# Performance work log

Measured on AMD Instinct MI355X. Metric: run time of the kernel, lower is better.

The kernel has to match this reference:

```python
import jax, jax.numpy as jnp
import numpy as np
from jax import lax

I, H, D1 = 130, 10, 20  # input_size, hidden_size, linear1 width


def _gru_last(x, Wih, Whh, bih, bhh):
    """PyTorch-convention GRU (gate order r,z,n); returns last hidden state [B,H]."""
    # Precompute input projections for all timesteps: [B,T,3H]
    xi = jnp.einsum('bti,gi->btg', x, Wih) + bih
    h0 = jnp.zeros((x.shape[0], H), x.dtype)

    def step(h, xt):  # xt: [B,3H]
        gh = h @ Whh.T + bhh  # [B,3H]
        r = jax.nn.sigmoid(xt[:, :H] + gh[:, :H])
        z = jax.nn.sigmoid(xt[:, H:2 * H] + gh[:, H:2 * H])
        n = jnp.tanh(xt[:, 2 * H:] + r * gh[:, 2 * H:])
        h_new = (1.0 - z) * n + z * h
        return h_new, None

    hT, _ = lax.scan(step, h0, jnp.swapaxes(xi, 0, 1))  # scan over time
    return hT


def setup_inputs() -> dict:
    key = jax.random.key(0)
    ks = jax.random.split(key, 12)
    B, T = 2048, 128
    s_ih = 1.0 / np.sqrt(H)
    inp = {
        'ru': jax.random.normal(ks[0], (B, T, I), jnp.float32),
        'en': jax.random.normal(ks[1], (B, T, I), jnp.float32),
        'ru_Wih': jax.random.uniform(ks[2], (3 * H, I), jnp.float32, -s_ih, s_ih),
        'ru_Whh': jax.random.uniform(ks[3], (3 * H, H), jnp.float32, -s_ih, s_ih),
        'ru_bih': jax.random.uniform(ks[4], (3 * H,), jnp.float32, -s_ih, s_ih),
        'ru_bhh': jax.random.uniform(ks[5], (3 * H,), jnp.float32, -s_ih, s_ih),
        'en_Wih': jax.random.uniform(ks[6], (3 * H, I), jnp.float32, -s_ih, s_ih),
        'en_Whh': jax.random.uniform(ks[7], (3 * H, H), jnp.float32, -s_ih, s_ih),
        'en_bih': jax.random.uniform(ks[8], (3 * H,), jnp.float32, -s_ih, s_ih),
        'en_bhh': jax.random.uniform(ks[9], (3 * H,), jnp.float32, -s_ih, s_ih),
        'W1': jax.random.uniform(ks[10], (D1, 2 * H), jnp.float32, -1 / np.sqrt(2 * H), 1 / np.sqrt(2 * H)),
        'b1': jnp.zeros((D1,), jnp.float32),
        'W2': jax.random.uniform(ks[11], (1, D1), jnp.float32, -1 / np.sqrt(D1), 1 / np.sqrt(D1)),
        'b2': jnp.zeros((1,), jnp.float32),
    }
    return inp


def reference(ru, en, ru_Wih, ru_Whh, ru_bih, ru_bhh,
              en_Wih, en_Whh, en_bih, en_bhh, W1, b1, W2, b2):
    ru_h = _gru_last(ru, ru_Wih, ru_Whh, ru_bih, ru_bhh)  # [B,H] (last timestep output)
    en_h = _gru_last(en, en_Wih, en_Whh, en_bih, en_bhh)  # [B,H]
    grus_out = jnp.concatenate([ru_h, en_h], axis=1)       # [B,2H]
    h1 = grus_out @ W1.T + b1                              # [B,20] (no activation in original)
    out = h1 @ W2.T + b2                                   # [B,1]
    return out
```

## Files before the change

### kernel.cpp

```cpp
#include <hip/hip_runtime.h>
#include <hip/hip_bf16.h>


#define BB 2048
#define TT 128
#define II 130
#define ROWS_PER_GRU (BB * TT)
#define ROWS_TOTAL   (2 * ROWS_PER_GRU)

typedef __attribute__((ext_vector_type(8))) short short8v;
typedef __attribute__((ext_vector_type(4))) float f32x4;

__device__ __forceinline__ float sigmoidf_fast(float x) {
    return __fdividef(1.f, 1.f + __expf(-x));
}
__device__ __forceinline__ float tanhf_fast(float x) {
    float ax = fabsf(x);
    float e = __expf(-2.f * ax);
    float t = __fdividef(1.f - e, 1.f + e);
    return copysignf(t, x);
}

__device__ __forceinline__ void split2(float x0, float x1,
                                       unsigned& hi, unsigned& lo) {
    unsigned u0 = __float_as_uint(x0), u1 = __float_as_uint(x1);
    hi = (u0 >> 16) | (u1 & 0xffff0000u);
    float f0 = __uint_as_float(u0 & 0xffff0000u);
    float f1 = __uint_as_float(u1 & 0xffff0000u);
    unsigned l0 = __float_as_uint(x0 - f0);
    unsigned l1 = __float_as_uint(x1 - f1);
    lo = (l0 >> 16) | (l1 & 0xffff0000u);
}

union U8 { unsigned u[4]; short8v v; };

__device__ __forceinline__ void load_split(const float* __restrict__ p,
                                           short8v& hi, short8v& lo) {
    U8 H, L;
    #pragma unroll
    for (int i = 0; i < 4; ++i) {
        const float2 xy = *(const float2*)(p + 2 * i);
        split2(xy.x, xy.y, H.u[i], L.u[i]);
    }
    hi = H.v; lo = L.v;
}

__global__ __launch_bounds__(256)
void xi_gemm(const float* __restrict__ ru, const float* __restrict__ en,
             const float* __restrict__ ruWih, const float* __restrict__ rubih,
             const float* __restrict__ enWih, const float* __restrict__ enbih,
             float* __restrict__ xi)
{
    const int tid  = threadIdx.x;
    const int lane = tid & 63;
    const int lr   = lane & 15;
    const int lk   = lane >> 4;
    const int w    = blockIdx.x * 4 + (tid >> 6);
    const int gru  = (w >= 4096);
    const long row0 = (long)(w & 4095) * 64;

    const float* __restrict__ X   = gru ? en    : ru;
    const float* __restrict__ Wf  = gru ? enWih : ruWih;
    const float* __restrict__ bih = gru ? enbih : rubih;

    short8v Bhi[2][4], Blo[2][4];
    float biasv[2], wt0[2], wt1[2];
    #pragma unroll
    for (int t = 0; t < 2; ++t) {
        const int g = 16 * t + lr;
        const int gv = (g < 30) ? g : 0;
        #pragma unroll
        for (int q = 0; q < 4; ++q)
            load_split(Wf + (long)gv * II + 32 * q + 8 * lk, Bhi[t][q], Blo[t][q]);
        if (g >= 30) {
            const short8v z = {0, 0, 0, 0, 0, 0, 0, 0};
            #pragma unroll
            for (int q = 0; q < 4; ++q) { Bhi[t][q] = z; Blo[t][q] = z; }
        }
        biasv[t] = bih[gv];
        const float2 wt = *(const float2*)(Wf + (long)gv * II + 128);
        wt0[t] = wt.x; wt1[t] = wt.y;
    }

    f32x4 acc[4][2];
    #pragma unroll
    for (int m = 0; m < 4; ++m)
        #pragma unroll
        for (int t = 0; t < 2; ++t)
            acc[m][t] = (f32x4){biasv[t], biasv[t], biasv[t], biasv[t]};

    #pragma unroll
    for (int m = 0; m < 4; ++m) {
        const float* __restrict__ xr = X + (row0 + 16 * m + lr) * (long)II;
        #pragma unroll
        for (int q = 0; q < 4; ++q) {
            short8v ahi, alo;
            load_split(xr + 32 * q + 8 * lk, ahi, alo);
            acc[m][0] = __builtin_amdgcn_mfma_f32_16x16x32_bf16(ahi, Bhi[0][q], acc[m][0], 0, 0, 0);
            acc[m][0] = __builtin_amdgcn_mfma_f32_16x16x32_bf16(ahi, Blo[0][q], acc[m][0], 0, 0, 0);
            acc[m][0] = __builtin_amdgcn_mfma_f32_16x16x32_bf16(alo, Bhi[0][q], acc[m][0], 0, 0, 0);
            acc[m][1] = __builtin_amdgcn_mfma_f32_16x16x32_bf16(ahi, Bhi[1][q], acc[m][1], 0, 0, 0);
            acc[m][1] = __builtin_amdgcn_mfma_f32_16x16x32_bf16(ahi, Blo[1][q], acc[m][1], 0, 0, 0);
            acc[m][1] = __builtin_amdgcn_mfma_f32_16x16x32_bf16(alo, Bhi[1][q], acc[m][1], 0, 0, 0);
        }
    }

    const long gb = (long)gru * ROWS_PER_GRU;
    #pragma unroll
    for (int m = 0; m < 4; ++m) {
        #pragma unroll
        for (int r = 0; r < 4; ++r) {
            const long rr = row0 + 16 * m + 4 * lk + r;
            const float2 xt = *(const float2*)(X + rr * (long)II + 128);
            float* __restrict__ xo = xi + (gb + rr) * 30;
            const float v0 = acc[m][0][r] + xt.x * wt0[0] + xt.y * wt1[0];
            xo[lr] = v0;
            if (lr < 14) {
                const float v1 = acc[m][1][r] + xt.x * wt0[1] + xt.y * wt1[1];
                xo[16 + lr] = v1;
            }
        }
    }
}

__global__ __launch_bounds__(256, 4)
void gru_scan(const float* __restrict__ xi,
              const float* __restrict__ ruWhh, const float* __restrict__ rubhh,
              const float* __restrict__ enWhh, const float* __restrict__ enbhh,
              const float* __restrict__ W1, const float* __restrict__ b1,
              const float* __restrict__ W2, const float* __restrict__ b2,
              float* __restrict__ out)
{
    const int tid  = threadIdx.x;
    const int wv   = tid >> 6;
    const int lane = tid & 63;
    const int c    = lane >> 5;
    const int k    = lane & 31;
    const int kq   = (k < 10) ? k : 0;
    const int chain = (blockIdx.x * 4 + wv) * 2 + c;
    const int gru   = chain >> 11;
    const int b     = chain & (BB - 1);

    const float* __restrict__ Whh = gru ? enWhh : ruWhh;
    const float* __restrict__ bhh = gru ? enbhh : rubhh;

    float whhR[10], whhZ[10], whhN[10];
    #pragma unroll
    for (int j = 0; j < 10; ++j) {
        whhR[j] = Whh[kq * 10 + j];
        whhZ[j] = Whh[(10 + kq) * 10 + j];
        whhN[j] = Whh[(20 + kq) * 10 + j];
    }
    const float bR = bhh[kq], bZ = bhh[10 + kq], bN = bhh[20 + kq];

    __shared__ __align__(16) float lds[4][32];
    float* __restrict__ H = lds[wv] + c * 16;
    if (k < 12) H[k] = 0.f;
    float hown = 0.f;

    const float* __restrict__ xrow =
        xi + ((long)gru * ROWS_PER_GRU + (long)b * TT) * 30;

    float xR0 = xrow[kq],      xZ0 = xrow[10 + kq],  xN0 = xrow[20 + kq];
    float xR1 = xrow[30 + kq], xZ1 = xrow[40 + kq],  xN1 = xrow[50 + kq];

    for (int t = 0; t < TT; ++t) {
        const float xR = xR0, xZ = xZ0, xN = xN0;
        xR0 = xR1; xZ0 = xZ1; xN0 = xN1;
        {
            const int tn = (t + 2 < TT) ? t + 2 : TT - 1;
            const float* __restrict__ xp = xrow + (long)tn * 30;
            xR1 = xp[kq]; xZ1 = xp[10 + kq]; xN1 = xp[20 + kq];
        }

        const float4 h03 = *(const float4*)(H);
        const float4 h47 = *(const float4*)(H + 4);
        const float2 h89 = *(const float2*)(H + 8);

        float gr = bR, gz = bZ, gn = bN;
        gr = fmaf(whhR[0], h03.x, gr); gz = fmaf(whhZ[0], h03.x, gz); gn = fmaf(whhN[0], h03.x, gn);
        gr = fmaf(whhR[1], h03.y, gr); gz = fmaf(whhZ[1], h03.y, gz); gn = fmaf(whhN[1], h03.y, gn);
        gr = fmaf(whhR[2], h03.z, gr); gz = fmaf(whhZ[2], h03.z, gz); gn = fmaf(whhN[2], h03.z, gn);
        gr = fmaf(whhR[3], h03.w, gr); gz = fmaf(whhZ[3], h03.w, gz); gn = fmaf(whhN[3], h03.w, gn);
        gr = fmaf(whhR[4], h47.x, gr); gz = fmaf(whhZ[4], h47.x, gz); gn = fmaf(whhN[4], h47.x, gn);
        gr = fmaf(whhR[5], h47.y, gr); gz = fmaf(whhZ[5], h47.y, gz); gn = fmaf(whhN[5], h47.y, gn);
        gr = fmaf(whhR[6], h47.z, gr); gz = fmaf(whhZ[6], h47.z, gz); gn = fmaf(whhN[6], h47.z, gn);
        gr = fmaf(whhR[7], h47.w, gr); gz = fmaf(whhZ[7], h47.w, gz); gn = fmaf(whhN[7], h47.w, gn);
        gr = fmaf(whhR[8], h89.x, gr); gz = fmaf(whhZ[8], h89.x, gz); gn = fmaf(whhN[8], h89.x, gn);
        gr = fmaf(whhR[9], h89.y, gr); gz = fmaf(whhZ[9], h89.y, gz); gn = fmaf(whhN[9], h89.y, gn);

        const float r = sigmoidf_fast(xR + gr);
        const float z = sigmoidf_fast(xZ + gz);
        const float n = tanhf_fast(xN + r * gn);
        const float hnew = fmaf(z, hown - n, n);
        hown = hnew;
        if (k < 10) H[k] = hnew;
    }

    float val = 0.f;
    if (k < 10) {
        float v = 0.f;
        #pragma unroll
        for (int d = 0; d < 20; ++d)
            v = fmaf(W2[d], W1[d * 20 + gru * 10 + k], v);
        val = v * hown;
        if (k == 0 && gru == 0) {
            float c0 = b2[0];
            #pragma unroll
            for (int d = 0; d < 20; ++d) c0 = fmaf(W2[d], b1[d], c0);
            val += c0;
        }
    }
    val += __shfl_xor(val, 8);
    val += __shfl_xor(val, 4);
    val += __shfl_xor(val, 2);
    val += __shfl_xor(val, 1);
    if (k == 0) atomicAdd(&out[b], val);
}

__global__ __launch_bounds__(256, 4)
void gru_fused(const float* __restrict__ ru, const float* __restrict__ en,
               const float* __restrict__ ruWih, const float* __restrict__ ruWhh,
               const float* __restrict__ rubih, const float* __restrict__ rubhh,
               const float* __restrict__ enWih, const float* __restrict__ enWhh,
               const float* __restrict__ enbih, const float* __restrict__ enbhh,
               const float* __restrict__ W1, const float* __restrict__ b1,
               const float* __restrict__ W2, const float* __restrict__ b2,
               float* __restrict__ out)
{
    const int tid  = threadIdx.x;
    const int wv   = tid >> 6;
    const int lane = tid & 63;
    const int g    = lane & 31;
    const int h    = lane >> 5;
    const int wid  = blockIdx.x * 4 + wv;
    const int gru  = wid >> 11;
    const int b    = wid & (BB - 1);

    const float* __restrict__ x   = gru ? en    : ru;
    const float* __restrict__ Wih = gru ? enWih : ruWih;
    const float* __restrict__ Whh = gru ? enWhh : ruWhh;
    const float* __restrict__ bih = gru ? enbih : rubih;
    const float* __restrict__ bhh = gru ? enbhh : rubhh;

    __shared__ __align__(16) float lds[4][176];
    float* __restrict__ X    = lds[wv];
    float* __restrict__ PRE  = X + 132;
    float* __restrict__ Hbuf = X + 164;

    const int gq = (g < 30) ? g : 0;
    float wih[64];
    #pragma unroll
    for (int j = 0; j < 64; ++j) wih[j] = Wih[gq * II + h * 64 + j];
    const float w_e = Wih[gq * II + 128 + h];
    float whh[10];
    #pragma unroll
    for (int k = 0; k < 10; ++k) whh[k] = Whh[gq * 10 + k];
    const float bihg = bih[gq];
    const float bhhg = bhh[gq];

    if (lane < 12) Hbuf[lane] = 0.f;
    float hown = 0.f;

    const float* __restrict__ xrow = x + (size_t)b * (TT * II);
    float xa = xrow[lane];
    float xb = xrow[64 + lane];
    float xc = (lane < 2) ? xrow[128 + lane] : 0.f;

    for (int t = 0; t < TT; ++t) {
        X[lane] = xa;
        X[64 + lane] = xb;
        if (lane < 2) X[128 + lane] = xc;
        {
            const int tn = (t < TT - 1) ? t + 1 : t;
            const float* __restrict__ xn = xrow + (size_t)tn * II;
            xa = xn[lane];
            xb = xn[64 + lane];
            xc = (lane < 2) ? xn[128 + lane] : 0.f;
        }
        const float4 h03 = *(const float4*)(Hbuf);
        const float4 h47 = *(const float4*)(Hbuf + 4);
        const float2 h89 = *(const float2*)(Hbuf + 8);
        float gh0 = fmaf(whh[0], h03.x, bhhg);
        float gh1 = whh[1] * h03.y;
        gh0 = fmaf(whh[2], h03.z, gh0);
        gh1 = fmaf(whh[3], h03.w, gh1);
        gh0 = fmaf(whh[4], h47.x, gh0);
        gh1 = fmaf(whh[5], h47.y, gh1);
        gh0 = fmaf(whh[6], h47.z, gh0);
        gh1 = fmaf(whh[7], h47.w, gh1);
        gh0 = fmaf(whh[8], h89.x, gh0);
        gh1 = fmaf(whh[9], h89.y, gh1);
        const float gh = gh0 + gh1;

        float s0 = 0.f, s1 = 0.f, s2 = 0.f, s3 = 0.f;
        const float4* __restrict__ xb4 = (const float4*)(X + h * 64);
        #pragma unroll
        for (int c = 0; c < 16; ++c) {
            const float4 v = xb4[c];
            s0 = fmaf(wih[4 * c + 0], v.x, s0);
            s1 = fmaf(wih[4 * c + 1], v.y, s1);
            s2 = fmaf(wih[4 * c + 2], v.z, s2);
            s3 = fmaf(wih[4 * c + 3], v.w, s3);
        }
        float s = (s0 + s1) + (s2 + s3);
        s = fmaf(w_e, X[128 + h], s);
        s += __shfl_xor(s, 32);

        const float xiv = s + bihg;
        const float pre = xiv + gh;
        if (lane < 30) PRE[lane] = pre;
        const float rpre = PRE[(g - 20) & 31];
        const float zpre = PRE[(g - 10) & 31];
        const float r = sigmoidf_fast(rpre);
        const float z = sigmoidf_fast(zpre);
        const float n = tanhf_fast(xiv + r * gh);
        const float hnew = (1.f - z) * n + z * hown;
        hown = hnew;
        if (lane >= 20 && lane < 30) Hbuf[lane - 20] = hnew;
    }

    float val = 0.f;
    if (lane < 10) {
        const float hk = Hbuf[lane];
        float v = 0.f;
        #pragma unroll
        for (int d = 0; d < 20; ++d)
            v = fmaf(W2[d], W1[d * 20 + gru * 10 + lane], v);
        val = v * hk;
        if (lane == 0 && gru == 0) {
            float c0 = b2[0];
            #pragma unroll
            for (int d = 0; d < 20; ++d) c0 = fmaf(W2[d], b1[d], c0);
            val += c0;
        }
    }
    #pragma unroll
    for (int o = 32; o > 0; o >>= 1) val += __shfl_xor(val, o);
    if (lane == 0) atomicAdd(&out[b], val);
}

extern "C" void kernel_launch(void* const* d_in, const int* in_sizes, int n_in,
                              void* d_out, int out_size, void* d_ws, size_t ws_size,
                              hipStream_t stream) {
    (void)in_sizes; (void)n_in;
    const float* ru    = (const float*)d_in[0];
    const float* en    = (const float*)d_in[1];
    const float* ruWih = (const float*)d_in[2];
    const float* ruWhh = (const float*)d_in[3];
    const float* rubih = (const float*)d_in[4];
    const float* rubhh = (const float*)d_in[5];
    const float* enWih = (const float*)d_in[6];
    const float* enWhh = (const float*)d_in[7];
    const float* enbih = (const float*)d_in[8];
    const float* enbhh = (const float*)d_in[9];
    const float* W1    = (const float*)d_in[10];
    const float* b1    = (const float*)d_in[11];
    const float* W2    = (const float*)d_in[12];
    const float* b2    = (const float*)d_in[13];
    float* out = (float*)d_out;

    hipMemsetAsync(d_out, 0, (size_t)out_size * sizeof(float), stream);

    const size_t xi_bytes = (size_t)ROWS_TOTAL * 30 * sizeof(float);
    if (ws_size >= xi_bytes) {
        float* xi = (float*)d_ws;
        xi_gemm<<<dim3(2048), dim3(256), 0, stream>>>(
            ru, en, ruWih, rubih, enWih, enbih, xi);
        gru_scan<<<dim3(512), dim3(256), 0, stream>>>(
            xi, ruWhh, rubhh, enWhh, enbhh, W1, b1, W2, b2, out);
    } else {
        gru_fused<<<dim3(1024), dim3(256), 0, stream>>>(
            ru, en, ruWih, ruWhh, rubih, rubhh,
            enWih, enWhh, enbih, enbhh, W1, b1, W2, b2, out);
    }
}
```

Baseline: 142.1 us.

## Stage input rows through LDS with coalesced float4 loads and register prefetch

The input-projection GEMM now copies each 16-row tile of X into per-wave shared memory using fully coalesced float4 loads, instead of reading strided 8-float chunks straight from global memory. The next tile is prefetched into registers while the current one is computed, so global latency overlaps with the MFMA work. Tail columns are also read from LDS. The cost is 33 KB of LDS per block, which may limit occupancy, and there is no barrier between the LDS writes and reads, so correctness relies on each wave only touching its own slice.

```diff
diff --git a/kernel.cpp b/kernel.cpp
--- a/kernel.cpp
+++ b/kernel.cpp
@@ -52,10 +52,11 @@
              float* __restrict__ xi)
 {
     const int tid  = threadIdx.x;
+    const int wv   = tid >> 6;
     const int lane = tid & 63;
     const int lr   = lane & 15;
     const int lk   = lane >> 4;
-    const int w    = blockIdx.x * 4 + (tid >> 6);
+    const int w    = blockIdx.x * 4 + wv;
     const int gru  = (w >= 4096);
     const long row0 = (long)(w & 4095) * 64;
 
@@ -82,41 +83,65 @@
         wt0[t] = wt.x; wt1[t] = wt.y;
     }
 
-    f32x4 acc[4][2];
-    #pragma unroll
-    for (int m = 0; m < 4; ++m)
-        #pragma unroll
-        for (int t = 0; t < 2; ++t)
-            acc[m][t] = (f32x4){biasv[t], biasv[t], biasv[t], biasv[t]};
-
-    #pragma unroll
-    for (int m = 0; m < 4; ++m) {
-        const float* __restrict__ xr = X + (row0 + 16 * m + lr) * (long)II;
+    __shared__ __align__(16) float lds[4][16 * II];
+    float4* __restrict__ L4 = (float4*)lds[wv];
+    const float* __restrict__ Lf = lds[wv];
+
+    const float4* __restrict__ src = (const float4*)X + row0 * (II / 2) / 2;
+
+    const long gb = (long)gru * ROWS_PER_GRU;
+
+    float4 pf0, pf1, pf2, pf3, pf4, pf5, pf6, pf7, pft;
+    {
+        const float4* __restrict__ s = src;
+        pf0 = s[lane];        pf1 = s[64 + lane];
+        pf2 = s[128 + lane];  pf3 = s[192 + lane];
+        pf4 = s[256 + lane];  pf5 = s[320 + lane];
+        pf6 = s[384 + lane];  pf7 = s[448 + lane];
+        if (lane < 8) pft = s[512 + lane];
+    }
+
+    #pragma unroll
+    for (int t = 0; t < 4; ++t) {
+        L4[lane]       = pf0;  L4[64 + lane]  = pf1;
+        L4[128 + lane] = pf2;  L4[192 + lane] = pf3;
+        L4[256 + lane] = pf4;  L4[320 + lane] = pf5;
+        L4[384 + lane] = pf6;  L4[448 + lane] = pf7;
+        if (lane < 8) L4[512 + lane] = pft;
+
+        if (t < 3) {
+            const float4* __restrict__ s = src + 520 * (t + 1);
+            pf0 = s[lane];        pf1 = s[64 + lane];
+            pf2 = s[128 + lane];  pf3 = s[192 + lane];
+            pf4 = s[256 + lane];  pf5 = s[320 + lane];
+            pf6 = s[384 + lane];  pf7 = s[448 + lane];
+            if (lane < 8) pft = s[512 + lane];
+        }
+
+        f32x4 a0 = (f32x4){biasv[0], biasv[0], biasv[0], biasv[0]};
+        f32x4 a1 = (f32x4){biasv[1], biasv[1], biasv[1], biasv[1]};
         #pragma unroll
         for (int q = 0; q < 4; ++q) {
             short8v ahi, alo;
-            load_split(xr + 32 * q + 8 * lk, ahi, alo);
-            acc[m][0] = __builtin_amdgcn_mfma_f32_16x16x32_bf16(ahi, Bhi[0][q], acc[m][0], 0, 0, 0);
-            acc[m][0] = __builtin_amdgcn_mfma_f32_16x16x32_bf16(ahi, Blo[0][q], acc[m][0], 0, 0, 0);
-            acc[m][0] = __builtin_amdgcn_mfma_f32_16x16x32_bf16(alo, Bhi[0][q], acc[m][0], 0, 0, 0);
-            acc[m][1] = __builtin_amdgcn_mfma_f32_16x16x32_bf16(ahi, Bhi[1][q], acc[m][1], 0, 0, 0);
-            acc[m][1] = __builtin_amdgcn_mfma_f32_16x16x32_bf16(ahi, Blo[1][q], acc[m][1], 0, 0, 0);
-            acc[m][1] = __builtin_amdgcn_mfma_f32_16x16x32_bf16(alo, Bhi[1][q], acc[m][1], 0, 0, 0);
-        }
-    }
-
-    const long gb = (long)gru * ROWS_PER_GRU;
-    #pragma unroll
-    for (int m = 0; m < 4; ++m) {
+            load_split(Lf + lr * II + 32 * q + 8 * lk, ahi, alo);
+            a0 = __builtin_amdgcn_mfma_f32_16x16x32_bf16(ahi, Bhi[0][q], a0, 0, 0, 0);
+            a0 = __builtin_amdgcn_mfma_f32_16x16x32_bf16(ahi, Blo[0][q], a0, 0, 0, 0);
+            a0 = __builtin_amdgcn_mfma_f32_16x16x32_bf16(alo, Bhi[0][q], a0, 0, 0, 0);
+            a1 = __builtin_amdgcn_mfma_f32_16x16x32_bf16(ahi, Bhi[1][q], a1, 0, 0, 0);
+            a1 = __builtin_amdgcn_mfma_f32_16x16x32_bf16(ahi, Blo[1][q], a1, 0, 0, 0);
+            a1 = __builtin_amdgcn_mfma_f32_16x16x32_bf16(alo, Bhi[1][q], a1, 0, 0, 0);
+        }
+
         #pragma unroll
         for (int r = 0; r < 4; ++r) {
-            const long rr = row0 + 16 * m + 4 * lk + r;
-            const float2 xt = *(const float2*)(X + rr * (long)II + 128);
+            const int rowin = 4 * lk + r;
+            const float2 xt = *(const float2*)(Lf + rowin * II + 128);
+            const long rr = row0 + 16 * t + rowin;
             float* __restrict__ xo = xi + (gb + rr) * 30;
-            const float v0 = acc[m][0][r] + xt.x * wt0[0] + xt.y * wt1[0];
+            const float v0 = a0[r] + xt.x * wt0[0] + xt.y * wt1[0];
             xo[lr] = v0;
             if (lr < 14) {
-                const float v1 = acc[m][1][r] + xt.x * wt0[1] + xt.y * wt1[1];
+                const float v1 = a1[r] + xt.x * wt0[1] + xt.y * wt1[1];
                 xo[16 + lr] = v1;
             }
         }
```

Result: faster. 118.6 us (-16.5%).

## Precompute split Wih MFMA fragments and shrink xi_gemm tiles to 16 rows

Applied to the files above, without the earlier changes.

Adds a tiny prep kernel that splits the Wih weights into bf16 hi/lo MFMA fragments once and stores them in the workspace. xi_gemm then loads ready-made fragments instead of re-splitting weights in every wave. Each wave now handles 16 rows instead of 64, with all A loads issued up front, and the grid grows to 8192 blocks to give more parallelism and latency hiding. The cost is an extra kernel launch and more blocks that each reload the fragments and bias.

```diff
diff --git a/kernel.cpp b/kernel.cpp
--- a/kernel.cpp
+++ b/kernel.cpp
@@ -7,9 +7,14 @@
 #define II 130
 #define ROWS_PER_GRU (BB * TT)
 #define ROWS_TOTAL   (2 * ROWS_PER_GRU)
+#define XI_BYTES ((size_t)ROWS_TOTAL * 30 * sizeof(float))
+#define FRAG_U4_PER_GRU 1024
 
 typedef __attribute__((ext_vector_type(8))) short short8v;
 typedef __attribute__((ext_vector_type(4))) float f32x4;
+
+union U8 { unsigned u[4]; short8v v; };
+union SU { uint4 u; short8v v; };
 
 __device__ __forceinline__ float sigmoidf_fast(float x) {
     return __fdividef(1.f, 1.f + __expf(-x));
@@ -32,8 +37,6 @@
     lo = (l0 >> 16) | (l1 & 0xffff0000u);
 }
 
-union U8 { unsigned u[4]; short8v v; };
-
 __device__ __forceinline__ void load_split(const float* __restrict__ p,
                                            short8v& hi, short8v& lo) {
     U8 H, L;
@@ -44,82 +47,125 @@
     }
     hi = H.v; lo = L.v;
 }
+
+__device__ __forceinline__ void split4(const float2* a,
+                                       short8v& hi, short8v& lo) {
+    U8 H, L;
+    #pragma unroll
+    for (int i = 0; i < 4; ++i) split2(a[i].x, a[i].y, H.u[i], L.u[i]);
+    hi = H.v; lo = L.v;
+}
+
+__global__ void prep_w(const float* __restrict__ ruWih,
+                       const float* __restrict__ enWih,
+                       uint4* __restrict__ frags)
+{
+    const int tid  = threadIdx.x;
+    const int gru  = tid >> 6;
+    const int lane = tid & 63;
+    const int lr   = lane & 15;
+    const int lk   = lane >> 4;
+    const float* __restrict__ Wf = gru ? enWih : ruWih;
+    uint4* __restrict__ fb = frags + gru * FRAG_U4_PER_GRU;
+    #pragma unroll
+    for (int t = 0; t < 2; ++t) {
+        const int g  = 16 * t + lr;
+        const int gv = (g < 30) ? g : 0;
+        #pragma unroll
+        for (int q = 0; q < 4; ++q) {
+            short8v hi, lo;
+            load_split(Wf + (long)gv * II + 32 * q + 8 * lk, hi, lo);
+            if (g >= 30) {
+                const short8v z = {0,0,0,0,0,0,0,0};
+                hi = z; lo = z;
+            }
+            SU sh, sl; sh.v = hi; sl.v = lo;
+            fb[((t * 4 + q) * 2 + 0) * 64 + lane] = sh.u;
+            fb[((t * 4 + q) * 2 + 1) * 64 + lane] = sl.u;
+        }
+    }
+}
+
+#define MFMA16(A, B, C) __builtin_amdgcn_mfma_f32_16x16x32_bf16((A), (B), (C), 0, 0, 0)
 
 __global__ __launch_bounds__(256)
 void xi_gemm(const float* __restrict__ ru, const float* __restrict__ en,
              const float* __restrict__ ruWih, const float* __restrict__ rubih,
              const float* __restrict__ enWih, const float* __restrict__ enbih,
-             float* __restrict__ xi)
+             const uint4* __restrict__ frags, float* __restrict__ xi)
 {
     const int tid  = threadIdx.x;
+    const int wv   = tid >> 6;
     const int lane = tid & 63;
     const int lr   = lane & 15;
     const int lk   = lane >> 4;
-    const int w    = blockIdx.x * 4 + (tid >> 6);
-    const int gru  = (w >= 4096);
-    const long row0 = (long)(w & 4095) * 64;
+    const int w    = blockIdx.x * 4 + wv;
+    const int gru  = (w >= 16384);
+    const long row0 = (long)(w & 16383) * 16;
 
     const float* __restrict__ X   = gru ? en    : ru;
     const float* __restrict__ Wf  = gru ? enWih : ruWih;
     const float* __restrict__ bih = gru ? enbih : rubih;
-
+    const float* __restrict__ xb  = X + row0 * II;
+
+    const float* __restrict__ arow = xb + (long)lr * II + 8 * lk;
+    float2 A0[4], A1[4], A2[4], A3[4];
+    #pragma unroll
+    for (int j = 0; j < 4; ++j) A0[j] = *(const float2*)(arow +  0 + 2 * j);
+    #pragma unroll
+    for (int j = 0; j < 4; ++j) A1[j] = *(const float2*)(arow + 32 + 2 * j);
+    #pragma unroll
+    for (int j = 0; j < 4; ++j) A2[j] = *(const float2*)(arow + 64 + 2 * j);
+    #pragma unroll
+    for (int j = 0; j < 4; ++j) A3[j] = *(const float2*)(arow + 96 + 2 * j);
+    float2 tl[4];
+    #pragma unroll
+    for (int r = 0; r < 4; ++r)
+        tl[r] = *(const float2*)(xb + (long)(4 * lk + r) * II + 128);
+
+    const uint4* __restrict__ fb = frags + gru * FRAG_U4_PER_GRU;
     short8v Bhi[2][4], Blo[2][4];
-    float biasv[2], wt0[2], wt1[2];
-    #pragma unroll
-    for (int t = 0; t < 2; ++t) {
-        const int g = 16 * t + lr;
-        const int gv = (g < 30) ? g : 0;
-        #pragma unroll
-        for (int q = 0; q < 4; ++q)
-            load_split(Wf + (long)gv * II + 32 * q + 8 * lk, Bhi[t][q], Blo[t][q]);
-        if (g >= 30) {
-            const short8v z = {0, 0, 0, 0, 0, 0, 0, 0};
-            #pragma unroll
-            for (int q = 0; q < 4; ++q) { Bhi[t][q] = z; Blo[t][q] = z; }
-        }
-        biasv[t] = bih[gv];
-        const float2 wt = *(const float2*)(Wf + (long)gv * II + 128);
-        wt0[t] = wt.x; wt1[t] = wt.y;
-    }
-
-    f32x4 acc[4][2];
-    #pragma unroll
-    for (int m = 0; m < 4; ++m)
-        #pragma unroll
-        for (int t = 0; t < 2; ++t)
-            acc[m][t] = (f32x4){biasv[t], biasv[t], biasv[t], biasv[t]};
-
-    #pragma unroll
-    for (int m = 0; m < 4; ++m) {
-        const float* __restrict__ xr = X + (row0 + 16 * m + lr) * (long)II;
+    #pragma unroll
+    for (int t = 0; t < 2; ++t)
         #pragma unroll
         for (int q = 0; q < 4; ++q) {
-            short8v ahi, alo;
-            load_split(xr + 32 * q + 8 * lk, ahi, alo);
-            acc[m][0] = __builtin_amdgcn_mfma_f32_16x16x32_bf16(ahi, Bhi[0][q], acc[m][0], 0, 0, 0);
-            acc[m][0] = __builtin_amdgcn_mfma_f32_16x16x32_bf16(ahi, Blo[0][q], acc[m][0], 0, 0, 0);
-            acc[m][0] = __builtin_amdgcn_mfma_f32_16x16x32_bf16(alo, Bhi[0][q], acc[m][0], 0, 0, 0);
-            acc[m][1] = __builtin_amdgcn_mfma_f32_16x16x32_bf16(ahi, Bhi[1][q], acc[m][1], 0, 0, 0);
-            acc[m][1] = __builtin_amdgcn_mfma_f32_16x16x32_bf16(ahi, Blo[1][q], acc[m][1], 0, 0, 0);
-            acc[m][1] = __builtin_amdgcn_mfma_f32_16x16x32_bf16(alo, Bhi[1][q], acc[m][1], 0, 0, 0);
-        }
-    }
+            SU sh, sl;
+            sh.u = fb[((t * 4 + q) * 2 + 0) * 64 + lane];
+            sl.u = fb[((t * 4 + q) * 2 + 1) * 64 + lane];
+            Bhi[t][q] = sh.v; Blo[t][q] = sl.v;
+        }
+
+    const int gv1 = (16 + lr < 30) ? 16 + lr : 0;
+    const float bias0 = bih[lr];
+    const float bias1 = bih[gv1];
+    const float2 w0 = *(const float2*)(Wf + (long)lr  * II + 128);
+    const float2 w1 = *(const float2*)(Wf + (long)gv1 * II + 128);
+
+    f32x4 a0 = (f32x4){bias0, bias0, bias0, bias0};
+    f32x4 a1 = (f32x4){bias1, bias1, bias1, bias1};
+
+    short8v ahi, alo;
+    split4(A0, ahi, alo);
+    a0 = MFMA16(ahi, Bhi[0][0], a0); a0 = MFMA16(ahi, Blo[0][0], a0); a0 = MFMA16(alo, Bhi[0][0], a0);
+    a1 = MFMA16(ahi, Bhi[1][0], a1); a1 = MFMA16(ahi, Blo[1][0], a1); a1 = MFMA16(alo, Bhi[1][0], a1);
+    split4(A1, ahi, alo);
+    a0 = MFMA16(ahi, Bhi[0][1], a0); a0 = MFMA16(ahi, Blo[0][1], a0); a0 = MFMA16(alo, Bhi[0][1], a0);
+    a1 = MFMA16(ahi, Bhi[1][1], a1); a1 = MFMA16(ahi, Blo[1][1], a1); a1 = MFMA16(alo, Bhi[1][1], a1);
+    split4(A2, ahi, alo);
+    a0 = MFMA16(ahi, Bhi[0][2], a0); a0 = MFMA16(ahi, Blo[0][2], a0); a0 = MFMA16(alo, Bhi[0][2], a0);
+    a1 = MFMA16(ahi, Bhi[1][2], a1); a1 = MFMA16(ahi, Blo[1][2], a1); a1 = MFMA16(alo, Bhi[1][2], a1);
+    split4(A3, ahi, alo);
+    a0 = MFMA16(ahi, Bhi[0][3], a0); a0 = MFMA16(ahi, Blo[0][3], a0); a0 = MFMA16(alo, Bhi[0][3], a0);
+    a1 = MFMA16(ahi, Bhi[1][3], a1); a1 = MFMA16(ahi, Blo[1][3], a1); a1 = MFMA16(alo, Bhi[1][3], a1);
 
     const long gb = (long)gru * ROWS_PER_GRU;
     #pragma unroll
-    for (int m = 0; m < 4; ++m) {
-        #pragma unroll
-        for (int r = 0; r < 4; ++r) {
-            const long rr = row0 + 16 * m + 4 * lk + r;
-            const float2 xt = *(const float2*)(X + rr * (long)II + 128);
-            float* __restrict__ xo = xi + (gb + rr) * 30;
-            const float v0 = acc[m][0][r] + xt.x * wt0[0] + xt.y * wt1[0];
-            xo[lr] = v0;
-            if (lr < 14) {
-                const float v1 = acc[m][1][r] + xt.x * wt0[1] + xt.y * wt1[1];
-                xo[16 + lr] = v1;
-            }
-        }
+    for (int r = 0; r < 4; ++r) {
+        const long rr = row0 + 4 * lk + r;
+        float* __restrict__ xo = xi + (gb + rr) * 30;
+        xo[lr] = a0[r] + tl[r].x * w0.x + tl[r].y * w0.y;
+        if (lr < 14)
+            xo[16 + lr] = a1[r] + tl[r].x * w1.x + tl[r].y * w1.y;
     }
 }
 
@@ -192,9 +238,8 @@
         const float r = sigmoidf_fast(xR + gr);
         const float z = sigmoidf_fast(xZ + gz);
         const float n = tanhf_fast(xN + r * gn);
-        const float hnew = fmaf(z, hown - n, n);
-        hown = hnew;
-        if (k < 10) H[k] = hnew;
+        hown = fmaf(z, hown - n, n);
+        if (k < 10) H[k] = hown;
     }
 
     float val = 0.f;
@@ -362,11 +407,13 @@
 
     hipMemsetAsync(d_out, 0, (size_t)out_size * sizeof(float), stream);
 
-    const size_t xi_bytes = (size_t)ROWS_TOTAL * 30 * sizeof(float);
-    if (ws_size >= xi_bytes) {
+    const size_t frag_bytes = 2 * FRAG_U4_PER_GRU * sizeof(uint4);
+    if (ws_size >= XI_BYTES + frag_bytes) {
         float* xi = (float*)d_ws;
-        xi_gemm<<<dim3(2048), dim3(256), 0, stream>>>(
-            ru, en, ruWih, rubih, enWih, enbih, xi);
+        uint4* frags = (uint4*)((char*)d_ws + XI_BYTES);
+        prep_w<<<dim3(1), dim3(128), 0, stream>>>(ruWih, enWih, frags);
+        xi_gemm<<<dim3(8192), dim3(256), 0, stream>>>(
+            ru, en, ruWih, rubih, enWih, enbih, frags, xi);
         gru_scan<<<dim3(512), dim3(256), 0, stream>>>(
             xi, ruWhh, rubhh, enWhh, enbhh, W1, b1, W2, b2, out);
     } else {
```

New measurement: 151.9 us. +6.9%, slower.
